# Performance work log

Hardware: AMD Instinct MI355X
Metric: run time of the kernel (lower is better)

## Reference

```python
import jax, jax.numpy as jnp
import numpy as np

N_NODES = 100000
D = 256
N_TYPES = 4
E1 = 300000
E2 = 300000


def setup_inputs() -> dict:
    key = jax.random.key(0)
    ks = jax.random.split(key, 9)
    x = jax.random.normal(ks[0], (N_NODES, D), dtype=jnp.float32)
    hyperedge_index_s1 = jax.random.randint(ks[1], (2, E1 * 1), 0, N_NODES, dtype=jnp.int32)
    hyperedge_type_s1 = jax.random.randint(ks[2], (E1,), 0, N_TYPES, dtype=jnp.int32)
    hyperedge_index_s2 = jax.random.randint(ks[3], (2, E2 * 2), 0, N_NODES, dtype=jnp.int32)
    hyperedge_type_s2 = jax.random.randint(ks[4], (E2,), 0, N_TYPES, dtype=jnp.int32)
    # xavier_normal init for A: std = sqrt(2 / (fan_in + fan_out))
    A_s1 = jax.random.normal(ks[5], (N_TYPES, 1 * D, D), dtype=jnp.float32) * np.sqrt(2.0 / (D + D)).astype(np.float32)
    A_s2 = jax.random.normal(ks[6], (N_TYPES, 2 * D, D), dtype=jnp.float32) * np.sqrt(2.0 / (2 * D + D)).astype(np.float32)
    lim = 1.0 / np.sqrt(D)
    W_c = jax.random.uniform(ks[7], (D, D), minval=-lim, maxval=lim, dtype=jnp.float32)
    b_c = jax.random.uniform(ks[8], (D,), minval=-lim, maxval=lim, dtype=jnp.float32)
    return dict(x=x,
                hyperedge_index_s1=hyperedge_index_s1, hyperedge_type_s1=hyperedge_type_s1,
                hyperedge_index_s2=hyperedge_index_s2, hyperedge_type_s2=hyperedge_type_s2,
                A_s1=A_s1, A_s2=A_s2, W_c=W_c, b_c=b_c)


def _shape_agg(x, A, idx, etype, shape, n_nodes):
    """Per-hyperedge-shape gather -> per-type matmul -> normalize -> scatter-add."""
    d = x.shape[1]
    e = etype.shape[0]
    # concat the `shape` source node features per hyperedge: [E, shape*d]
    src = x[idx[0]].reshape(e, shape * d)
    # first target slot per hyperedge: [E]
    dst = idx[1].reshape(e, shape)[:, 0]
    agg = jnp.zeros((n_nodes, d), dtype=x.dtype)
    for t in range(A.shape[0]):  # small fixed number of edge types
        mask = etype == t
        tmp = src @ A[t]  # [E, d]
        # per-destination count within this (shape, type) group == torch.unique counts
        counts = jax.ops.segment_sum(mask.astype(x.dtype), dst, num_segments=n_nodes)
        norm = jnp.where(mask, 1.0 / jnp.maximum(counts[dst], 1.0), 0.0)
        agg = agg.at[dst].add(norm[:, None] * tmp)
    return agg


def reference(x, hyperedge_index_s1, hyperedge_type_s1,
              hyperedge_index_s2, hyperedge_type_s2,
              A_s1, A_s2, W_c, b_c):
    n = x.shape[0]
    agg = _shape_agg(x, A_s1, hyperedge_index_s1, hyperedge_type_s1, 1, n)
    agg = agg + _shape_agg(x, A_s2, hyperedge_index_s2, hyperedge_type_s2, 2, n)
    return x @ W_c.T + b_c + agg
```

## Files before the change

kernel.cpp:

```cpp
#include <hip/hip_runtime.h>
#include <stdint.h>

#define N_NODES 100000
#define D 256
#define NT 4

typedef float f32x4 __attribute__((ext_vector_type(4)));
typedef __bf16 bf16x8 __attribute__((ext_vector_type(8)));

__device__ __forceinline__ unsigned short f2bf(float f) {
    unsigned u = __float_as_uint(f);
    u += 0x7FFF + ((u >> 16) & 1);
    return (unsigned short)(u >> 16);
}

__device__ __forceinline__ void gload_lds16(const void* g, void* lds) {
    __builtin_amdgcn_global_load_lds(
        (const __attribute__((address_space(1))) unsigned int*)g,
        (__attribute__((address_space(3))) unsigned int*)lds, 16, 0, 0);
}


template<int SHAPE>
__global__ void k_count(const int* __restrict__ idx, const int* __restrict__ etype,
                        int E, int* __restrict__ counts) {
    int e = blockIdx.x * 256 + threadIdx.x;
    if (e >= E) return;
    int t = etype[e];
    int dst = idx[(size_t)SHAPE * E + (size_t)SHAPE * e];
    atomicAdd(&counts[t * N_NODES + dst], 1);
}


__global__ __launch_bounds__(256) void k_scan1(const int* __restrict__ in, int n,
        int* __restrict__ outv, int* __restrict__ bsums) {
    __shared__ int s[256];
    int tid = threadIdx.x;
    int i = blockIdx.x * 1024 + tid * 4;
    int v0 = 0, v1 = 0, v2 = 0, v3 = 0;
    if (i + 3 < n) {
        int4 v = *(const int4*)(in + i);
        v0 = v.x; v1 = v.y; v2 = v.z; v3 = v.w;
    } else {
        if (i     < n) v0 = in[i];
        if (i + 1 < n) v1 = in[i + 1];
        if (i + 2 < n) v2 = in[i + 2];
        if (i + 3 < n) v3 = in[i + 3];
    }
    int tsum = v0 + v1 + v2 + v3;
    s[tid] = tsum; __syncthreads();
    for (int off = 1; off < 256; off <<= 1) {
        int t = (tid >= off) ? s[tid - off] : 0;
        __syncthreads();
        s[tid] += t;
        __syncthreads();
    }
    int excl = s[tid] - tsum;
    if (tid == 255) bsums[blockIdx.x] = s[255];
    int o0 = excl, o1 = o0 + v0, o2 = o1 + v1, o3 = o2 + v2;
    if (i + 3 < n) {
        *(int4*)(outv + i) = make_int4(o0, o1, o2, o3);
    } else {
        if (i     < n) outv[i]     = o0;
        if (i + 1 < n) outv[i + 1] = o1;
        if (i + 2 < n) outv[i + 2] = o2;
        if (i + 3 < n) outv[i + 3] = o3;
    }
}

__global__ void k_scan2(int* __restrict__ bsums, int nb) {
    __shared__ int s[512];
    int t = threadIdx.x;
    int v = (t < nb) ? bsums[t] : 0;
    s[t] = v; __syncthreads();
    for (int off = 1; off < 512; off <<= 1) {
        int u = (t >= off) ? s[t - off] : 0;
        __syncthreads();
        s[t] += u;
        __syncthreads();
    }
    if (t < nb) bsums[t] = s[t] - v;
}

__global__ __launch_bounds__(256) void k_scan3(int* __restrict__ cellofs,
        int* __restrict__ cellcur, const int* __restrict__ bsums, int n) {
    int i = blockIdx.x * 1024 + threadIdx.x * 4;
    int add = bsums[blockIdx.x];
    if (i + 3 < n) {
        int4 v = *(int4*)(cellofs + i);
        v.x += add; v.y += add; v.z += add; v.w += add;
        *(int4*)(cellofs + i) = v;
        *(int4*)(cellcur + i) = v;
    } else {
        for (int k = 0; k < 4; ++k)
            if (i + k < n) { int v = cellofs[i + k] + add; cellofs[i + k] = v; cellcur[i + k] = v; }
    }
}


template<int SHAPE>
__global__ void k_place(const int* __restrict__ idx, const int* __restrict__ etype, int E,
                        int* __restrict__ cellcur, int* __restrict__ bucket) {
    int e = blockIdx.x * 256 + threadIdx.x;
    if (e >= E) return;
    int t = etype[e];
    int dst = idx[(size_t)SHAPE * E + (size_t)SHAPE * e];
    int pos = atomicAdd(&cellcur[t * N_NODES + dst], 1);
    bucket[pos] = e;
}


__global__ __launch_bounds__(256) void k_cvt(const float* __restrict__ in,
        unsigned short* __restrict__ ob, int n8) {
    int i = blockIdx.x * 256 + threadIdx.x;
    if (i >= n8) return;
    const float4* p = (const float4*)in + (size_t)i * 2;
    float4 v0 = p[0], v1 = p[1];
    union { unsigned short us[8]; uint4 u4; } o;
    o.us[0] = f2bf(v0.x); o.us[1] = f2bf(v0.y); o.us[2] = f2bf(v0.z); o.us[3] = f2bf(v0.w);
    o.us[4] = f2bf(v1.x); o.us[5] = f2bf(v1.y); o.us[6] = f2bf(v1.z); o.us[7] = f2bf(v1.w);
    *(uint4*)(ob + (size_t)i * 8) = o.u4;
}


__global__ void k_cvt_At(const float* __restrict__ A, unsigned short* __restrict__ AT, int K) {
    __shared__ float tl[32][33];
    const float* Ab = A + (size_t)blockIdx.z * K * D;
    unsigned short* Ob = AT + (size_t)blockIdx.z * D * K;
    int k0 = blockIdx.x * 32, j0 = blockIdx.y * 32;
    int lx = threadIdx.x, ly = threadIdx.y;
    for (int yy = ly; yy < 32; yy += 8)
        tl[yy][lx] = Ab[(size_t)(k0 + yy) * D + j0 + lx];
    __syncthreads();
    for (int yy = ly; yy < 32; yy += 8)
        Ob[(size_t)(j0 + yy) * K + k0 + lx] = f2bf(tl[lx][yy]);
}


__global__ __launch_bounds__(256) void k_init_mfma(const unsigned short* __restrict__ xb,
        const unsigned short* __restrict__ Wb, const float* __restrict__ bias,
        float* __restrict__ out, int n) {
    __shared__ __align__(16) char xs[64 * 128];
    int row0 = blockIdx.x * 64;
    int tid = threadIdx.x;
    int lane = tid & 63, w = tid >> 6;
    int l15 = lane & 15, l4 = lane >> 4;
    f32x4 acc[4][4];
    #pragma unroll
    for (int m = 0; m < 4; ++m)
        #pragma unroll
        for (int nn = 0; nn < 4; ++nn) acc[m][nn] = (f32x4)0.f;

    for (int kk = 0; kk < D; kk += 64) {
        #pragma unroll
        for (int it = 0; it < 2; ++it) {
            int f = it * 256 + tid;
            int r = f >> 3, q0 = f & 7;
            int q = q0 ^ (r & 7);
            int gr = row0 + r; if (gr >= n) gr = n - 1;
            gload_lds16(xb + (size_t)gr * D + kk + q * 8, xs + f * 16);
        }
        bf16x8 bfr[2][4];
        #pragma unroll
        for (int ks = 0; ks < 2; ++ks)
            #pragma unroll
            for (int nn = 0; nn < 4; ++nn) {
                int j = w * 64 + nn * 16 + l15;
                int k = kk + ks * 32 + l4 * 8;
                bfr[ks][nn] = *(const bf16x8*)(Wb + (size_t)j * D + k);
            }
        __syncthreads();
        #pragma unroll
        for (int ks = 0; ks < 2; ++ks)
            #pragma unroll
            for (int m = 0; m < 4; ++m) {
                int R = m * 16 + l15;
                int C = ks * 4 + l4;
                bf16x8 a = *(const bf16x8*)(xs + R * 128 + ((C ^ (R & 7)) << 4));
                #pragma unroll
                for (int nn = 0; nn < 4; ++nn)
                    acc[m][nn] = __builtin_amdgcn_mfma_f32_16x16x32_bf16(
                        a, bfr[ks][nn], acc[m][nn], 0, 0, 0);
            }
        __syncthreads();
    }
    #pragma unroll
    for (int m = 0; m < 4; ++m)
        #pragma unroll
        for (int nn = 0; nn < 4; ++nn) {
            int col = w * 64 + nn * 16 + l15;
            float bv = bias[col];
            #pragma unroll
            for (int r = 0; r < 4; ++r) {
                int row = row0 + m * 16 + l4 * 4 + r;
                if (row < n) out[(size_t)row * D + col] = acc[m][nn][r] + bv;
            }
        }
}


template<int SHAPE, int SCR>
__global__ __launch_bounds__(256) void k_edge_mfma(const unsigned short* __restrict__ xb,
        const int* __restrict__ idx, const unsigned short* __restrict__ AT,
        float* __restrict__ out, unsigned short* __restrict__ eo, int E,
        const int* __restrict__ counts, const int* __restrict__ cellofs,
        const int* __restrict__ bucket) {
    constexpr int K = SHAPE * 256;
    __shared__ __align__(16) char xs[64 * 128];
    __shared__ int srcS[SHAPE][64];
    __shared__ int dstS[64];
    __shared__ float normS[64];

    int t = blockIdx.y;
    int offs_t = cellofs[t * N_NODES];
    int end_t = (t == NT - 1) ? E : cellofs[(t + 1) * N_NODES];
    int cnt = end_t - offs_t;
    int tile = blockIdx.x * 64;
    if (tile >= cnt) return;
    int nE = min(64, cnt - tile);
    int base = offs_t + tile;
    int tid = threadIdx.x;

    if (tid < 64) {
        bool valid = tid < nE;
        int e = bucket[base + (valid ? tid : 0)];
        int dst = idx[(size_t)SHAPE * E + (size_t)SHAPE * e];
        dstS[tid] = dst;
        int c = counts[t * N_NODES + dst];
        normS[tid] = valid ? 1.0f / (float)(c > 1 ? c : 1) : 0.0f;
        srcS[0][tid] = idx[SHAPE * e];
        if (SHAPE == 2) srcS[SHAPE - 1][tid] = idx[SHAPE * e + SHAPE - 1];
    }
    __syncthreads();

    const unsigned short* Bt = AT + (size_t)t * D * K;
    int lane = tid & 63, w = tid >> 6;
    int l15 = lane & 15, l4 = lane >> 4;
    f32x4 acc[4][4];
    #pragma unroll
    for (int m = 0; m < 4; ++m)
        #pragma unroll
        for (int nn = 0; nn < 4; ++nn) acc[m][nn] = (f32x4)0.f;

    for (int kk = 0; kk < K; kk += 64) {
        #pragma unroll
        for (int it = 0; it < 2; ++it) {
            int f = it * 256 + tid;
            int r = f >> 3, q0 = f & 7;
            int q = q0 ^ (r & 7);
            int node = srcS[SHAPE == 2 ? (kk >> 8) : 0][r];
            int col = (kk & 255) + q * 8;
            gload_lds16(xb + (size_t)node * D + col, xs + f * 16);
        }
        bf16x8 bfr[2][4];
        #pragma unroll
        for (int ks = 0; ks < 2; ++ks)
            #pragma unroll
            for (int nn = 0; nn < 4; ++nn) {
                int j = w * 64 + nn * 16 + l15;
                int k = kk + ks * 32 + l4 * 8;
                bfr[ks][nn] = *(const bf16x8*)(Bt + (size_t)j * K + k);
            }
        __syncthreads();
        #pragma unroll
        for (int ks = 0; ks < 2; ++ks)
            #pragma unroll
            for (int m = 0; m < 4; ++m) {
                int R = m * 16 + l15;
                int C = ks * 4 + l4;
                bf16x8 a = *(const bf16x8*)(xs + R * 128 + ((C ^ (R & 7)) << 4));
                #pragma unroll
                for (int nn = 0; nn < 4; ++nn)
                    acc[m][nn] = __builtin_amdgcn_mfma_f32_16x16x32_bf16(
                        a, bfr[ks][nn], acc[m][nn], 0, 0, 0);
            }
        __syncthreads();
    }

    if constexpr (SCR) {
        __shared__ unsigned short re[64][264];
        #pragma unroll
        for (int m = 0; m < 4; ++m)
            #pragma unroll
            for (int r = 0; r < 4; ++r) {
                int rr = m * 16 + l4 * 4 + r;
                float nm = normS[rr];
                #pragma unroll
                for (int nn = 0; nn < 4; ++nn) {
                    int col = w * 64 + nn * 16 + l15;
                    re[rr][col] = f2bf(nm * acc[m][nn][r]);
                }
            }
        __syncthreads();
        #pragma unroll
        for (int it = 0; it < 8; ++it) {
            int f = it * 256 + tid;
            int row = f >> 5, seg = f & 31;
            if (row < nE) {
                uint4 v = *(const uint4*)&re[row][seg * 8];
                *(uint4*)(eo + (size_t)(base + row) * D + seg * 8) = v;
            }
        }
    } else {
        #pragma unroll
        for (int m = 0; m < 4; ++m)
            #pragma unroll
            for (int r = 0; r < 4; ++r) {
                int rr = m * 16 + l4 * 4 + r;
                if (rr < nE) {
                    float nm = normS[rr];
                    size_t ob = (size_t)dstS[rr] * D;
                    #pragma unroll
                    for (int nn = 0; nn < 4; ++nn) {
                        int col = w * 64 + nn * 16 + l15;
                        atomicAdd(&out[ob + col], nm * acc[m][nn][r]);
                    }
                }
            }
    }
}


__global__ __launch_bounds__(256) void k_reduce(const unsigned short* __restrict__ eo,
        const int* __restrict__ counts, const int* __restrict__ cellofs,
        float* __restrict__ out) {
    int wv = threadIdx.x >> 6, lane = threadIdx.x & 63;
    int dst = blockIdx.x * 4 + wv;
    if (dst >= N_NODES) return;
    float a0 = 0.f, a1 = 0.f, a2 = 0.f, a3 = 0.f;
    int tot = 0;
    #pragma unroll
    for (int t = 0; t < NT; ++t) {
        int start = cellofs[t * N_NODES + dst];
        int c = counts[t * N_NODES + dst];
        tot += c;
        for (int i = 0; i < c; ++i) {
            const unsigned short* row = eo + (size_t)(start + i) * D + lane * 4;
            uint2 v = *(const uint2*)row;
            a0 += __uint_as_float(v.x << 16);
            a1 += __uint_as_float(v.x & 0xFFFF0000u);
            a2 += __uint_as_float(v.y << 16);
            a3 += __uint_as_float(v.y & 0xFFFF0000u);
        }
    }
    if (tot) {
        float4* o = (float4*)&out[(size_t)dst * D + lane * 4];
        float4 cur = *o;
        cur.x += a0; cur.y += a1; cur.z += a2; cur.w += a3;
        *o = cur;
    }
}


extern "C" void kernel_launch(void* const* d_in, const int* in_sizes, int n_in,
                              void* d_out, int out_size, void* d_ws, size_t ws_size,
                              hipStream_t stream) {
    const float* x  = (const float*)d_in[0];
    const int* idx1 = (const int*)d_in[1];
    const int* ty1  = (const int*)d_in[2];
    const int* idx2 = (const int*)d_in[3];
    const int* ty2  = (const int*)d_in[4];
    const float* A1 = (const float*)d_in[5];
    const float* A2 = (const float*)d_in[6];
    const float* W  = (const float*)d_in[7];
    const float* b  = (const float*)d_in[8];
    float* out = (float*)d_out;

    int E1 = in_sizes[2];
    int E2 = in_sizes[4];
    int maxE = E1 > E2 ? E1 : E2;
    const int NCELL = NT * N_NODES;
    const int NB = (NCELL + 1023) / 1024;
    const int NRB = (N_NODES + 3) / 4;

    char* p = (char*)d_ws;
    unsigned short* xb  = (unsigned short*)p; p += (size_t)N_NODES * D * 2;
    unsigned short* Wb  = (unsigned short*)p; p += (size_t)D * D * 2;
    unsigned short* A1T = (unsigned short*)p; p += (size_t)NT * D * 256 * 2;
    unsigned short* A2T = (unsigned short*)p; p += (size_t)NT * D * 512 * 2;
    int* counts  = (int*)p; p += (size_t)NCELL * 4;
    int* cellofs = (int*)p; p += (size_t)NCELL * 4;
    int* cellcur = (int*)p; p += (size_t)NCELL * 4;
    int* bsums   = (int*)p; p += 512 * 4;
    int* bucket  = (int*)p; p += (size_t)maxE * 4;
    unsigned short* eo = (unsigned short*)p; p += (size_t)maxE * D * 2;
    bool scr = ((size_t)(p - (char*)d_ws)) <= ws_size;

    k_cvt<<<(N_NODES * D / 8 + 255) / 256, 256, 0, stream>>>(x, xb, N_NODES * D / 8);
    k_cvt<<<(D * D / 8 + 255) / 256, 256, 0, stream>>>(W, Wb, D * D / 8);
    k_cvt_At<<<dim3(256 / 32, D / 32, NT), dim3(32, 8), 0, stream>>>(A1, A1T, 256);
    k_cvt_At<<<dim3(512 / 32, D / 32, NT), dim3(32, 8), 0, stream>>>(A2, A2T, 512);

    k_init_mfma<<<(N_NODES + 63) / 64, 256, 0, stream>>>(xb, Wb, b, out, N_NODES);

    hipMemsetAsync(counts, 0, (size_t)NCELL * sizeof(int), stream);
    k_count<1><<<(E1 + 255) / 256, 256, 0, stream>>>(idx1, ty1, E1, counts);
    k_scan1<<<NB, 256, 0, stream>>>(counts, NCELL, cellofs, bsums);
    k_scan2<<<1, 512, 0, stream>>>(bsums, NB);
    k_scan3<<<NB, 256, 0, stream>>>(cellofs, cellcur, bsums, NCELL);
    k_place<1><<<(E1 + 255) / 256, 256, 0, stream>>>(idx1, ty1, E1, cellcur, bucket);
    if (scr) {
        k_edge_mfma<1, 1><<<dim3((E1 + 63) / 64, NT), 256, 0, stream>>>(
            xb, idx1, A1T, out, eo, E1, counts, cellofs, bucket);
        k_reduce<<<NRB, 256, 0, stream>>>(eo, counts, cellofs, out);
    } else {
        k_edge_mfma<1, 0><<<dim3((E1 + 63) / 64, NT), 256, 0, stream>>>(
            xb, idx1, A1T, out, nullptr, E1, counts, cellofs, bucket);
    }

    hipMemsetAsync(counts, 0, (size_t)NCELL * sizeof(int), stream);
    k_count<2><<<(E2 + 255) / 256, 256, 0, stream>>>(idx2, ty2, E2, counts);
    k_scan1<<<NB, 256, 0, stream>>>(counts, NCELL, cellofs, bsums);
    k_scan2<<<1, 512, 0, stream>>>(bsums, NB);
    k_scan3<<<NB, 256, 0, stream>>>(cellofs, cellcur, bsums, NCELL);
    k_place<2><<<(E2 + 255) / 256, 256, 0, stream>>>(idx2, ty2, E2, cellcur, bucket);
    if (scr) {
        k_edge_mfma<2, 1><<<dim3((E2 + 63) / 64, NT), 256, 0, stream>>>(
            xb, idx2, A2T, out, eo, E2, counts, cellofs, bucket);
        k_reduce<<<NRB, 256, 0, stream>>>(eo, counts, cellofs, out);
    } else {
        k_edge_mfma<2, 0><<<dim3((E2 + 63) / 64, NT), 256, 0, stream>>>(
            xb, idx2, A2T, out, nullptr, E2, counts, cellofs, bucket);
    }
}
```

Before: 640.2 us.

## Merge both shape reductions into one pass and halve epilogue LDS staging

Keeps separate counts, offsets and bf16 scratch buffers for the two hyperedge shapes, so a single reduce kernel can sum both shapes' per-edge outputs and update each output row once instead of twice. The edge kernel's epilogue stages results through a half-size LDS buffer in two passes, which should raise occupancy, and it uses nontemporal stores. The reduce reads scratch with nontemporal loads. In exchange it needs more workspace, and falls back to the old path when the workspace is too small.

```diff
diff --git a/kernel.cpp b/kernel.cpp
--- a/kernel.cpp
+++ b/kernel.cpp
@@ -7,6 +7,8 @@
 
 typedef float f32x4 __attribute__((ext_vector_type(4)));
 typedef __bf16 bf16x8 __attribute__((ext_vector_type(8)));
+typedef unsigned int uint32x4 __attribute__((ext_vector_type(4)));
+typedef unsigned int uint32x2 __attribute__((ext_vector_type(2)));
 
 __device__ __forceinline__ unsigned short f2bf(float f) {
     unsigned u = __float_as_uint(f);
@@ -207,6 +209,7 @@
         const int* __restrict__ bucket) {
     constexpr int K = SHAPE * 256;
     __shared__ __align__(16) char xs[64 * 128];
+    __shared__ unsigned short re[32][264];
     __shared__ int srcS[SHAPE][64];
     __shared__ int dstS[64];
     __shared__ float normS[64];
@@ -278,27 +281,35 @@
     }
 
     if constexpr (SCR) {
-        __shared__ unsigned short re[64][264];
-        #pragma unroll
-        for (int m = 0; m < 4; ++m)
-            #pragma unroll
-            for (int r = 0; r < 4; ++r) {
-                int rr = m * 16 + l4 * 4 + r;
-                float nm = normS[rr];
+        #pragma unroll
+        for (int half = 0; half < 2; ++half) {
+            if (half) __syncthreads();
+            #pragma unroll
+            for (int mi = 0; mi < 2; ++mi) {
+                int m = half * 2 + mi;
                 #pragma unroll
-                for (int nn = 0; nn < 4; ++nn) {
-                    int col = w * 64 + nn * 16 + l15;
-                    re[rr][col] = f2bf(nm * acc[m][nn][r]);
+                for (int r = 0; r < 4; ++r) {
+                    int rr = m * 16 + l4 * 4 + r;
+                    float nm = normS[rr];
+                    int rl = rr - half * 32;
+                    #pragma unroll
+                    for (int nn = 0; nn < 4; ++nn) {
+                        int col = w * 64 + nn * 16 + l15;
+                        re[rl][col] = f2bf(nm * acc[m][nn][r]);
+                    }
                 }
             }
-        __syncthreads();
-        #pragma unroll
-        for (int it = 0; it < 8; ++it) {
-            int f = it * 256 + tid;
-            int row = f >> 5, seg = f & 31;
-            if (row < nE) {
-                uint4 v = *(const uint4*)&re[row][seg * 8];
-                *(uint4*)(eo + (size_t)(base + row) * D + seg * 8) = v;
+            __syncthreads();
+            #pragma unroll
+            for (int it = 0; it < 4; ++it) {
+                int f = it * 256 + tid;
+                int row = f >> 5, seg = f & 31;
+                int grow = half * 32 + row;
+                if (grow < nE) {
+                    uint32x4 v = *(const uint32x4*)&re[row][seg * 8];
+                    __builtin_nontemporal_store(v,
+                        (uint32x4*)(eo + (size_t)(base + grow) * D + seg * 8));
+                }
             }
         }
     } else {
@@ -321,7 +332,26 @@
 }
 
 
-__global__ __launch_bounds__(256) void k_reduce(const unsigned short* __restrict__ eo,
+__device__ __forceinline__ void acc_runs(const unsigned short* __restrict__ eo,
+        const int* __restrict__ counts, const int* __restrict__ cellofs,
+        int dst, int lane, float& a0, float& a1, float& a2, float& a3, int& tot) {
+    #pragma unroll
+    for (int t = 0; t < NT; ++t) {
+        int start = cellofs[t * N_NODES + dst];
+        int c = counts[t * N_NODES + dst];
+        tot += c;
+        for (int i = 0; i < c; ++i) {
+            const uint32x2* row = (const uint32x2*)(eo + (size_t)(start + i) * D + lane * 4);
+            uint32x2 v = __builtin_nontemporal_load(row);
+            a0 += __uint_as_float(v.x << 16);
+            a1 += __uint_as_float(v.x & 0xFFFF0000u);
+            a2 += __uint_as_float(v.y << 16);
+            a3 += __uint_as_float(v.y & 0xFFFF0000u);
+        }
+    }
+}
+
+__global__ __launch_bounds__(256) void k_reduce_one(const unsigned short* __restrict__ eo,
         const int* __restrict__ counts, const int* __restrict__ cellofs,
         float* __restrict__ out) {
     int wv = threadIdx.x >> 6, lane = threadIdx.x & 63;
@@ -329,20 +359,26 @@
     if (dst >= N_NODES) return;
     float a0 = 0.f, a1 = 0.f, a2 = 0.f, a3 = 0.f;
     int tot = 0;
-    #pragma unroll
-    for (int t = 0; t < NT; ++t) {
-        int start = cellofs[t * N_NODES + dst];
-        int c = counts[t * N_NODES + dst];
-        tot += c;
-        for (int i = 0; i < c; ++i) {
-            const unsigned short* row = eo + (size_t)(start + i) * D + lane * 4;
-            uint2 v = *(const uint2*)row;
-            a0 += __uint_as_float(v.x << 16);
-            a1 += __uint_as_float(v.x & 0xFFFF0000u);
-            a2 += __uint_as_float(v.y << 16);
-            a3 += __uint_as_float(v.y & 0xFFFF0000u);
-        }
-    }
+    acc_runs(eo, counts, cellofs, dst, lane, a0, a1, a2, a3, tot);
+    if (tot) {
+        float4* o = (float4*)&out[(size_t)dst * D + lane * 4];
+        float4 cur = *o;
+        cur.x += a0; cur.y += a1; cur.z += a2; cur.w += a3;
+        *o = cur;
+    }
+}
+
+__global__ __launch_bounds__(256) void k_reduce_two(
+        const unsigned short* __restrict__ eo1, const int* __restrict__ c1, const int* __restrict__ o1,
+        const unsigned short* __restrict__ eo2, const int* __restrict__ c2, const int* __restrict__ o2,
+        float* __restrict__ out) {
+    int wv = threadIdx.x >> 6, lane = threadIdx.x & 63;
+    int dst = blockIdx.x * 4 + wv;
+    if (dst >= N_NODES) return;
+    float a0 = 0.f, a1 = 0.f, a2 = 0.f, a3 = 0.f;
+    int tot = 0;
+    acc_runs(eo1, c1, o1, dst, lane, a0, a1, a2, a3, tot);
+    acc_runs(eo2, c2, o2, dst, lane, a0, a1, a2, a3, tot);
     if (tot) {
         float4* o = (float4*)&out[(size_t)dst * D + lane * 4];
         float4 cur = *o;
@@ -378,13 +414,18 @@
     unsigned short* Wb  = (unsigned short*)p; p += (size_t)D * D * 2;
     unsigned short* A1T = (unsigned short*)p; p += (size_t)NT * D * 256 * 2;
     unsigned short* A2T = (unsigned short*)p; p += (size_t)NT * D * 512 * 2;
-    int* counts  = (int*)p; p += (size_t)NCELL * 4;
-    int* cellofs = (int*)p; p += (size_t)NCELL * 4;
+    int* counts1 = (int*)p; p += (size_t)NCELL * 4;
+    int* cellofs1= (int*)p; p += (size_t)NCELL * 4;
+    int* counts2 = (int*)p; p += (size_t)NCELL * 4;
+    int* cellofs2= (int*)p; p += (size_t)NCELL * 4;
     int* cellcur = (int*)p; p += (size_t)NCELL * 4;
     int* bsums   = (int*)p; p += 512 * 4;
     int* bucket  = (int*)p; p += (size_t)maxE * 4;
-    unsigned short* eo = (unsigned short*)p; p += (size_t)maxE * D * 2;
-    bool scr = ((size_t)(p - (char*)d_ws)) <= ws_size;
+    unsigned short* eo1 = (unsigned short*)p; p += (size_t)maxE * D * 2;
+    size_t need1 = (size_t)(p - (char*)d_ws);
+    unsigned short* eo2 = (unsigned short*)p; p += (size_t)maxE * D * 2;
+    size_t need2 = (size_t)(p - (char*)d_ws);
+    int mode = (need2 <= ws_size) ? 2 : (need1 <= ws_size) ? 1 : 0;
 
     k_cvt<<<(N_NODES * D / 8 + 255) / 256, 256, 0, stream>>>(x, xb, N_NODES * D / 8);
     k_cvt<<<(D * D / 8 + 255) / 256, 256, 0, stream>>>(W, Wb, D * D / 8);
@@ -393,33 +434,39 @@
 
     k_init_mfma<<<(N_NODES + 63) / 64, 256, 0, stream>>>(xb, Wb, b, out, N_NODES);
 
-    hipMemsetAsync(counts, 0, (size_t)NCELL * sizeof(int), stream);
-    k_count<1><<<(E1 + 255) / 256, 256, 0, stream>>>(idx1, ty1, E1, counts);
-    k_scan1<<<NB, 256, 0, stream>>>(counts, NCELL, cellofs, bsums);
+    hipMemsetAsync(counts1, 0, (size_t)NCELL * sizeof(int), stream);
+    k_count<1><<<(E1 + 255) / 256, 256, 0, stream>>>(idx1, ty1, E1, counts1);
+    k_scan1<<<NB, 256, 0, stream>>>(counts1, NCELL, cellofs1, bsums);
     k_scan2<<<1, 512, 0, stream>>>(bsums, NB);
-    k_scan3<<<NB, 256, 0, stream>>>(cellofs, cellcur, bsums, NCELL);
+    k_scan3<<<NB, 256, 0, stream>>>(cellofs1, cellcur, bsums, NCELL);
     k_place<1><<<(E1 + 255) / 256, 256, 0, stream>>>(idx1, ty1, E1, cellcur, bucket);
-    if (scr) {
+    if (mode) {
         k_edge_mfma<1, 1><<<dim3((E1 + 63) / 64, NT), 256, 0, stream>>>(
-            xb, idx1, A1T, out, eo, E1, counts, cellofs, bucket);
-        k_reduce<<<NRB, 256, 0, stream>>>(eo, counts, cellofs, out);
+            xb, idx1, A1T, out, eo1, E1, counts1, cellofs1, bucket);
+        if (mode == 1)
+            k_reduce_one<<<NRB, 256, 0, stream>>>(eo1, counts1, cellofs1, out);
     } else {
         k_edge_mfma<1, 0><<<dim3((E1 + 63) / 64, NT), 256, 0, stream>>>(
-            xb, idx1, A1T, out, nullptr, E1, counts, cellofs, bucket);
-    }
-
-    hipMemsetAsync(counts, 0, (size_t)NCELL * sizeof(int), stream);
-    k_count<2><<<(E2 + 255) / 256, 256, 0, stream>>>(idx2, ty2, E2, counts);
-    k_scan1<<<NB, 256, 0, stream>>>(counts, NCELL, cellofs, bsums);
+            xb, idx1, A1T, out, nullptr, E1, counts1, cellofs1, bucket);
+    }
+
+    hipMemsetAsync(counts2, 0, (size_t)NCELL * sizeof(int), stream);
+    k_count<2><<<(E2 + 255) / 256, 256, 0, stream>>>(idx2, ty2, E2, counts2);
+    k_scan1<<<NB, 256, 0, stream>>>(counts2, NCELL, cellofs2, bsums);
     k_scan2<<<1, 512, 0, stream>>>(bsums, NB);
-    k_scan3<<<NB, 256, 0, stream>>>(cellofs, cellcur, bsums, NCELL);
+    k_scan3<<<NB, 256, 0, stream>>>(cellofs2, cellcur, bsums, NCELL);
     k_place<2><<<(E2 + 255) / 256, 256, 0, stream>>>(idx2, ty2, E2, cellcur, bucket);
-    if (scr) {
+    if (mode) {
+        unsigned short* eoS2 = (mode == 2) ? eo2 : eo1;
         k_edge_mfma<2, 1><<<dim3((E2 + 63) / 64, NT), 256, 0, stream>>>(
-            xb, idx2, A2T, out, eo, E2, counts, cellofs, bucket);
-        k_reduce<<<NRB, 256, 0, stream>>>(eo, counts, cellofs, out);
+            xb, idx2, A2T, out, eoS2, E2, counts2, cellofs2, bucket);
+        if (mode == 2)
+            k_reduce_two<<<NRB, 256, 0, stream>>>(eo1, counts1, cellofs1,
+                                                  eo2, counts2, cellofs2, out);
+        else
+            k_reduce_one<<<NRB, 256, 0, stream>>>(eo1, counts2, cellofs2, out);
     } else {
         k_edge_mfma<2, 0><<<dim3((E2 + 63) / 64, NT), 256, 0, stream>>>(
-            xb, idx2, A2T, out, nullptr, E2, counts, cellofs, bucket);
-    }
-}
+            xb, idx2, A2T, out, nullptr, E2, counts2, cellofs2, bucket);
+    }
+}
```

Measured after the change: 607.7 us. -5.1%, faster.
